# Optimization experiments

Measured on AMD Instinct MI355X. Metric: run time of the kernel, lower is better.

## Reference

```python
import jax, jax.numpy as jnp
import numpy as np

H, W = 1024, 2048      # dims from __init__
C = 34                 # Cityscapes label ids 0..33 (thing classes 24..33)
N_INST = 128           # instance capacity (len(instance_probs))


def setup_inputs() -> dict:
    key = jax.random.key(0)
    k1, k2, k3, k4 = jax.random.split(key, 4)
    return {
        "segmentation_map": jax.random.randint(k1, (H, W), 0, C, dtype=jnp.int32),
        "instance_maps": jax.random.randint(k2, (H, W), 0, N_INST + 1, dtype=jnp.int32),
        "seg_map_probs": jax.random.uniform(k3, (C, H, W), dtype=jnp.float32),
        "instance_probs": jax.random.uniform(k4, (N_INST,), dtype=jnp.float32),
    }


def reference(segmentation_map, instance_maps, seg_map_probs, instance_probs):
    # nn.Threshold(23.99, 50): x if x > 23.99 else 50; then things = (thresh <= 33)
    seg_f = segmentation_map.astype(jnp.float32)
    things = (seg_f > 23.99) & (seg_f <= 33.0)           # (H, W) bool
    inst = jnp.where(things, instance_maps, 0)            # zero-out non-thing pixels

    flat_inst = inst.reshape(-1)                          # (HW,)
    flat_seg = segmentation_map.reshape(-1)               # (HW,)

    # segmented histogram: pixel counts per (instance, class)
    pair_idx = flat_inst * C + flat_seg
    counts2d = jax.ops.segment_sum(
        jnp.ones_like(flat_inst), pair_idx, num_segments=(N_INST + 1) * C
    ).reshape(N_INST + 1, C)

    # segmented sum of every class prob map over each instance mask
    probs_pix = seg_map_probs.reshape(C, -1).T            # (HW, C)
    sums2d = jax.ops.segment_sum(probs_pix, flat_inst, num_segments=N_INST + 1)  # (N+1, C)

    counts = counts2d[1:]                                 # drop background id 0 -> (N, C)
    sums = sums2d[1:]                                     # (N, C)

    inst_class = jnp.argmax(counts, axis=1).astype(jnp.int32)     # mode class per instance
    total = counts.sum(axis=1)                                     # seg_counts.sum()
    # mean of the winning class's prob map over the instance mask
    seg_prob = jnp.take_along_axis(sums, inst_class[:, None], axis=1)[:, 0] / jnp.maximum(
        total, 1
    ).astype(seg_map_probs.dtype)

    # per-instance binary masks, uint8 like the torch code
    inst_ids = jnp.arange(1, N_INST + 1, dtype=inst.dtype)
    inst_masks = (inst[None, :, :] == inst_ids[:, None, None]).astype(jnp.uint8)  # (N, H, W)

    valid = total > 0   # which instance slots actually appear in the image
    return inst_masks, inst_class, instance_probs, seg_prob, total, valid
```

## Files before the change

### kernel.cpp

```cpp
#include <hip/hip_runtime.h>

#define HH   1024
#define WW   2048
#define HWP  (HH * WW)
#define CC   34
#define NI   128
#define THING_LO 24
#define THING_HI 33
#define NTC  10

typedef float nfloat4 __attribute__((ext_vector_type(4)));

#define OFF_CLASS  ((size_t)NI * HWP)
#define OFF_PROBS  (OFF_CLASS + NI)
#define OFF_SEGP   (OFF_PROBS + NI)
#define OFF_TOTAL  (OFF_SEGP + NI)
#define OFF_VALID  (OFF_TOTAL + NI)

#define WS_COUNTS  0
#define WS_CLS     (NI * NTC * 4)
#define WS_INV     (WS_CLS + NI * 4)
#define WS_INST    8192

__device__ __forceinline__ int thing_inst(int s, int im) {
    return (s >= THING_LO && s <= THING_HI) ? im : 0;
}

__global__ __launch_bounds__(256) void k0_prep(
    const int* __restrict__ seg, const int* __restrict__ imap,
    unsigned int* __restrict__ inst_pack, int* __restrict__ counts)
{
    const int t = blockIdx.x * 256 + threadIdx.x;
    const int p = t * 4;
    const int4 sg = *reinterpret_cast<const int4*>(seg + p);
    const int4 im = *reinterpret_cast<const int4*>(imap + p);

    const int i0 = thing_inst(sg.x, im.x);
    const int i1 = thing_inst(sg.y, im.y);
    const int i2 = thing_inst(sg.z, im.z);
    const int i3 = thing_inst(sg.w, im.w);

    inst_pack[t] = (unsigned)i0 | ((unsigned)i1 << 8) |
                   ((unsigned)i2 << 16) | ((unsigned)i3 << 24);

    if (i0 > 0) atomicAdd(&counts[(i0 - 1) * NTC + (sg.x - THING_LO)], 1);
    if (i1 > 0) atomicAdd(&counts[(i1 - 1) * NTC + (sg.y - THING_LO)], 1);
    if (i2 > 0) atomicAdd(&counts[(i2 - 1) * NTC + (sg.z - THING_LO)], 1);
    if (i3 > 0) atomicAdd(&counts[(i3 - 1) * NTC + (sg.w - THING_LO)], 1);
}

__global__ __launch_bounds__(128) void k2_stats(
    const int* __restrict__ counts, const float* __restrict__ iprobs,
    float* __restrict__ out, int* __restrict__ cls_ws, float* __restrict__ inv_ws)
{
    const int i = threadIdx.x;
    int bestv = 0, bestc = 0, tot = 0;
    #pragma unroll
    for (int j = 0; j < NTC; ++j) {
        const int c = counts[i * NTC + j];
        tot += c;
        if (c > bestv) { bestv = c; bestc = THING_LO + j; }
    }
    cls_ws[i] = bestc;
    inv_ws[i] = 1.0f / (float)(tot > 0 ? tot : 1);
    out[OFF_CLASS + i] = (float)bestc;
    out[OFF_PROBS + i] = iprobs[i];
    out[OFF_SEGP  + i] = 0.0f;
    out[OFF_TOTAL + i] = (float)tot;
    out[OFF_VALID + i] = (tot > 0) ? 1.0f : 0.0f;
}

#define MCHUNK_PX 32768
#define MCHUNKS   (HWP / MCHUNK_PX)
__global__ __launch_bounds__(256) void k_mask(
    const unsigned int* __restrict__ inst_pack, float* __restrict__ out)
{
    const int plane = blockIdx.x >> 6;
    const int chunk = blockIdx.x & 63;
    const unsigned pid = (unsigned)(plane + 1);
    const size_t base_px = (size_t)chunk * MCHUNK_PX;
    float* oplane = out + (size_t)plane * HWP + base_px;
    const unsigned int* ip = inst_pack + (base_px >> 2);

    #pragma unroll 8
    for (int j = 0; j < MCHUNK_PX / (256 * 4); ++j) {
        const int q = j * 256 + threadIdx.x;
        const unsigned int w = ip[q];
        nfloat4 v;
        v.x = ((w & 255u)         == pid) ? 1.0f : 0.0f;
        v.y = (((w >> 8) & 255u)  == pid) ? 1.0f : 0.0f;
        v.z = (((w >> 16) & 255u) == pid) ? 1.0f : 0.0f;
        v.w = ((w >> 24)          == pid) ? 1.0f : 0.0f;
        __builtin_nontemporal_store(v, reinterpret_cast<nfloat4*>(oplane + q * 4));
    }
}

__global__ __launch_bounds__(256) void k3_segsum(
    const unsigned int* __restrict__ inst_pack, const float* __restrict__ probs,
    const int* __restrict__ cls_ws, const float* __restrict__ inv_ws,
    float* __restrict__ out)
{
    __shared__ float lsum[NI];
    __shared__ int   scls[NI];
    if (threadIdx.x < NI) {
        lsum[threadIdx.x] = 0.0f;
        scls[threadIdx.x] = cls_ws[threadIdx.x];
    }
    __syncthreads();

    const int t = blockIdx.x * 256 + threadIdx.x;
    const uint4 wv = reinterpret_cast<const uint4*>(inst_pack)[t];
    const int base_px = t * 16;
    const unsigned wvs[4] = { wv.x, wv.y, wv.z, wv.w };
    #pragma unroll
    for (int wi = 0; wi < 4; ++wi) {
        const unsigned w = wvs[wi];
        #pragma unroll
        for (int k = 0; k < 4; ++k) {
            const int inst = (int)((w >> (8 * k)) & 255u);
            if (inst > 0) {
                const size_t idx = (size_t)scls[inst - 1] * HWP +
                                   (size_t)(base_px + wi * 4 + k);
                atomicAdd(&lsum[inst - 1], probs[idx]);
            }
        }
    }
    __syncthreads();
    if (threadIdx.x < NI) {
        const float v = lsum[threadIdx.x];
        if (v != 0.0f)
            atomicAdd(&out[OFF_SEGP + threadIdx.x], v * inv_ws[threadIdx.x]);
    }
}

extern "C" void kernel_launch(void* const* d_in, const int* in_sizes, int n_in,
                              void* d_out, int out_size, void* d_ws, size_t ws_size,
                              hipStream_t stream) {
    const int*   seg    = (const int*)d_in[0];
    const int*   imap   = (const int*)d_in[1];
    const float* probs  = (const float*)d_in[2];
    const float* iprobs = (const float*)d_in[3];
    float* out = (float*)d_out;

    char* ws = (char*)d_ws;
    int*          counts    = (int*)(ws + WS_COUNTS);
    int*          cls_ws    = (int*)(ws + WS_CLS);
    float*        inv_ws    = (float*)(ws + WS_INV);
    unsigned int* inst_pack = (unsigned int*)(ws + WS_INST);

    (void)hipMemsetAsync(counts, 0, NI * NTC * sizeof(int), stream);

    k0_prep<<<(HWP / 4) / 256, 256, 0, stream>>>(seg, imap, inst_pack, counts);
    k2_stats<<<1, 128, 0, stream>>>(counts, iprobs, out, cls_ws, inv_ws);
    k_mask<<<NI * MCHUNKS, 256, 0, stream>>>(inst_pack, out);
    k3_segsum<<<(HWP / 16) / 256, 256, 0, stream>>>(inst_pack, probs, cls_ws, inv_ws, out);
}
```

Before: 1.336 ms.

## Merge mask writer and segment-sum gather into one kernel launch

Replaces the separate mask kernel and segmented-sum kernel with a single launch. Its first 256 blocks run a grid-strided gather/sum and the remaining blocks write all 128 mask planes. Each mask thread now reads its packed instance word once and stores 128 strided float4s, where before each block handled one plane chunk. This removes a launch and lets the gather overlap with the mask writes. The cost is that each thread's store stream is strided by a full plane, which may hurt write coalescing and locality.

```diff
diff --git a/kernel.cpp b/kernel.cpp
--- a/kernel.cpp
+++ b/kernel.cpp
@@ -21,6 +21,10 @@
 #define WS_CLS     (NI * NTC * 4)
 #define WS_INV     (WS_CLS + NI * 4)
 #define WS_INST    8192
+
+#define GATHER_BLOCKS 256
+#define MASK_BLOCKS   ((HWP / 4) / 256)
+#define MERGED_BLOCKS (GATHER_BLOCKS + MASK_BLOCKS)
 
 __device__ __forceinline__ int thing_inst(int s, int im) {
     return (s >= THING_LO && s <= THING_HI) ? im : 0;
@@ -70,66 +74,65 @@
     out[OFF_VALID + i] = (tot > 0) ? 1.0f : 0.0f;
 }
 
-#define MCHUNK_PX 32768
-#define MCHUNKS   (HWP / MCHUNK_PX)
-__global__ __launch_bounds__(256) void k_mask(
-    const unsigned int* __restrict__ inst_pack, float* __restrict__ out)
-{
-    const int plane = blockIdx.x >> 6;
-    const int chunk = blockIdx.x & 63;
-    const unsigned pid = (unsigned)(plane + 1);
-    const size_t base_px = (size_t)chunk * MCHUNK_PX;
-    float* oplane = out + (size_t)plane * HWP + base_px;
-    const unsigned int* ip = inst_pack + (base_px >> 2);
-
-    #pragma unroll 8
-    for (int j = 0; j < MCHUNK_PX / (256 * 4); ++j) {
-        const int q = j * 256 + threadIdx.x;
-        const unsigned int w = ip[q];
-        nfloat4 v;
-        v.x = ((w & 255u)         == pid) ? 1.0f : 0.0f;
-        v.y = (((w >> 8) & 255u)  == pid) ? 1.0f : 0.0f;
-        v.z = (((w >> 16) & 255u) == pid) ? 1.0f : 0.0f;
-        v.w = ((w >> 24)          == pid) ? 1.0f : 0.0f;
-        __builtin_nontemporal_store(v, reinterpret_cast<nfloat4*>(oplane + q * 4));
-    }
-}
-
-__global__ __launch_bounds__(256) void k3_segsum(
+__global__ __launch_bounds__(256) void k_merged(
     const unsigned int* __restrict__ inst_pack, const float* __restrict__ probs,
     const int* __restrict__ cls_ws, const float* __restrict__ inv_ws,
     float* __restrict__ out)
 {
     __shared__ float lsum[NI];
     __shared__ int   scls[NI];
-    if (threadIdx.x < NI) {
-        lsum[threadIdx.x] = 0.0f;
-        scls[threadIdx.x] = cls_ws[threadIdx.x];
-    }
-    __syncthreads();
 
-    const int t = blockIdx.x * 256 + threadIdx.x;
-    const uint4 wv = reinterpret_cast<const uint4*>(inst_pack)[t];
-    const int base_px = t * 16;
-    const unsigned wvs[4] = { wv.x, wv.y, wv.z, wv.w };
-    #pragma unroll
-    for (int wi = 0; wi < 4; ++wi) {
-        const unsigned w = wvs[wi];
+    if (blockIdx.x >= GATHER_BLOCKS) {
+        const int t = (blockIdx.x - GATHER_BLOCKS) * 256 + threadIdx.x;
+        const unsigned w = inst_pack[t];
+        const int i0 = (int)(w & 255u);
+        const int i1 = (int)((w >> 8) & 255u);
+        const int i2 = (int)((w >> 16) & 255u);
+        const int i3 = (int)(w >> 24);
+
+        float* o = out + (size_t)t * 4;
         #pragma unroll
-        for (int k = 0; k < 4; ++k) {
-            const int inst = (int)((w >> (8 * k)) & 255u);
-            if (inst > 0) {
-                const size_t idx = (size_t)scls[inst - 1] * HWP +
-                                   (size_t)(base_px + wi * 4 + k);
-                atomicAdd(&lsum[inst - 1], probs[idx]);
+        for (int i = 1; i <= NI; ++i) {
+            nfloat4 v;
+            v.x = (i0 == i) ? 1.0f : 0.0f;
+            v.y = (i1 == i) ? 1.0f : 0.0f;
+            v.z = (i2 == i) ? 1.0f : 0.0f;
+            v.w = (i3 == i) ? 1.0f : 0.0f;
+            __builtin_nontemporal_store(v, reinterpret_cast<nfloat4*>(o));
+            o += HWP;
+        }
+    } else {
+        if (threadIdx.x < NI) {
+            lsum[threadIdx.x] = 0.0f;
+            scls[threadIdx.x] = cls_ws[threadIdx.x];
+        }
+        __syncthreads();
+
+        for (int t = blockIdx.x * 256 + threadIdx.x; t < HWP / 16;
+             t += GATHER_BLOCKS * 256) {
+            const uint4 wv = reinterpret_cast<const uint4*>(inst_pack)[t];
+            const int base_px = t * 16;
+            const unsigned wvs[4] = { wv.x, wv.y, wv.z, wv.w };
+            #pragma unroll
+            for (int wi = 0; wi < 4; ++wi) {
+                const unsigned w = wvs[wi];
+                #pragma unroll
+                for (int k = 0; k < 4; ++k) {
+                    const int inst = (int)((w >> (8 * k)) & 255u);
+                    if (inst > 0) {
+                        const size_t idx = (size_t)scls[inst - 1] * HWP +
+                                           (size_t)(base_px + wi * 4 + k);
+                        atomicAdd(&lsum[inst - 1], probs[idx]);
+                    }
+                }
             }
         }
-    }
-    __syncthreads();
-    if (threadIdx.x < NI) {
-        const float v = lsum[threadIdx.x];
-        if (v != 0.0f)
-            atomicAdd(&out[OFF_SEGP + threadIdx.x], v * inv_ws[threadIdx.x]);
+        __syncthreads();
+        if (threadIdx.x < NI) {
+            const float v = lsum[threadIdx.x];
+            if (v != 0.0f)
+                atomicAdd(&out[OFF_SEGP + threadIdx.x], v * inv_ws[threadIdx.x]);
+        }
     }
 }
 
@@ -152,6 +155,5 @@
 
     k0_prep<<<(HWP / 4) / 256, 256, 0, stream>>>(seg, imap, inst_pack, counts);
     k2_stats<<<1, 128, 0, stream>>>(counts, iprobs, out, cls_ws, inv_ws);
-    k_mask<<<NI * MCHUNKS, 256, 0, stream>>>(inst_pack, out);
-    k3_segsum<<<(HWP / 16) / 256, 256, 0, stream>>>(inst_pack, probs, cls_ws, inv_ws, out);
+    k_merged<<<MERGED_BLOCKS, 256, 0, stream>>>(inst_pack, probs, cls_ws, inv_ws, out);
 }
```

Measured after the change: 1.330 ms. No clear change (-0.5%).
